# Optimization experiments

Measured on AMD Instinct MI355X. Metric: run time of the kernel, lower is better.

## Reference

```python
import jax, jax.numpy as jnp
import numpy as np

ITERATIONS = 10
EPS = 1e-8
ALPHA = 1.0
BETA = 1.0


def _conv3x3x3(x):
    # all-ones 3x3x3 kernel, padding=1 (SAME), single channel; NCDHW layout
    k = jnp.ones((1, 1, 3, 3, 3), x.dtype)
    return jax.lax.conv_general_dilated(
        x, k, window_strides=(1, 1, 1), padding='SAME',
        dimension_numbers=('NCDHW', 'OIDHW', 'NCDHW'))


def _soft_skeletonize(x):
    x = jax.nn.sigmoid(x)
    skeleton = x
    for _ in range(ITERATIONS):
        eroded = (_conv3x3x3(skeleton) > 0).astype(x.dtype)
        opened = (_conv3x3x3(eroded) > 0).astype(x.dtype)
        skeleton = jnp.clip(skeleton - opened, 0.0, 1.0)
    return skeleton


def _count_components(binary):
    neighbors = _conv3x3x3(binary)
    mask = binary > 0
    cnt = jnp.sum(mask).astype(binary.dtype)
    # torch.mean(neighbors[mask] + eps) == sum((neighbors+eps)*mask)/cnt
    mean_nb = jnp.sum(jnp.where(mask, neighbors + EPS, 0.0)) / jnp.maximum(cnt, 1.0)
    return (cnt / mean_nb)[None]


def setup_inputs() -> dict:
    key = jax.random.key(0)
    k1, k2 = jax.random.split(key)
    pred = jax.random.normal(k1, (2, 1, 192, 192, 192), dtype=jnp.float32)
    target = jax.random.uniform(k2, (2, 1, 192, 192, 192), dtype=jnp.float32)
    return {"pred": pred, "target": target}


def reference(pred, target):
    pred_prob = jax.nn.sigmoid(pred)
    # NOTE: module applies sigmoid again inside _soft_skeletonize (faithful)
    pred_skeleton = _soft_skeletonize(pred_prob)
    target_skeleton = _soft_skeletonize(target)

    intersection = jnp.sum(pred_skeleton * target_skeleton)
    union = jnp.sum(pred_skeleton) + jnp.sum(target_skeleton)
    skeleton_loss = 1.0 - (2.0 * intersection + EPS) / (union + EPS)

    pred_binary = (pred_prob > 0.5).astype(pred.dtype)
    target_binary = target  # .float() no-op
    pred_components = _count_components(pred_binary)
    target_components = _count_components(target_binary)
    connectivity_loss = jnp.mean(jnp.abs(pred_components - target_components))

    return ALPHA * skeleton_loss + BETA * connectivity_loss
```

## Files before the change

kernel.cpp:

```cpp
#include <hip/hip_runtime.h>
#include <math.h>

#define NN 192
#define PLANE (NN * NN)
#define VOLSZ (NN * NN * NN)
#define ZC 24
#define SLABR 8
#define NSLAB (NN / SLABR)
#define SLOTF (10 * NN)
#define NBIN 8
#define EPSF 1e-8f

template <int MODE>
__device__ __forceinline__ float bval(float u) {
  return (MODE == 0) ? ((u > 0.f) ? 1.f : 0.f) : u;
}

#define GLOAD16(G, L)                                                       \
  __builtin_amdgcn_global_load_lds(                                         \
      (const __attribute__((address_space(1))) void*)(G),                   \
      (__attribute__((address_space(3))) void*)(L), 16, 0, 0)

struct PlaneR {
  float4 a, b, c, d;
};

template <int MODE>
__device__ __forceinline__ void consume2(const PlaneR& P, float mA, float mD, float mz,
                                         int lane, float4& sY, float4& sZ,
                                         float4& cY, float4& cZ) {
  const float a0 = bval<MODE>(P.a.x), a1 = bval<MODE>(P.a.y), a2 = bval<MODE>(P.a.z), a3 = bval<MODE>(P.a.w);
  const float b0 = bval<MODE>(P.b.x), b1 = bval<MODE>(P.b.y), b2 = bval<MODE>(P.b.z), b3 = bval<MODE>(P.b.w);
  const float c0 = bval<MODE>(P.c.x), c1 = bval<MODE>(P.c.y), c2 = bval<MODE>(P.c.z), c3 = bval<MODE>(P.c.w);
  const float d0 = bval<MODE>(P.d.x), d1 = bval<MODE>(P.d.y), d2 = bval<MODE>(P.d.z), d3 = bval<MODE>(P.d.w);
  const float u0 = b0 + c0, u1 = b1 + c1, u2 = b2 + c2, u3 = b3 + c3;
  const float tY0 = fmaf(a0, mA, u0), tY1 = fmaf(a1, mA, u1), tY2 = fmaf(a2, mA, u2), tY3 = fmaf(a3, mA, u3);
  const float tZ0 = fmaf(d0, mD, u0), tZ1 = fmaf(d1, mD, u1), tZ2 = fmaf(d2, mD, u2), tZ3 = fmaf(d3, mD, u3);
  const float upY = __shfl_up(tY3, 1), dnY = __shfl_down(tY0, 1);
  const float upZ = __shfl_up(tZ3, 1), dnZ = __shfl_down(tZ0, 1);
  const float tlY = (lane == 0) ? 0.f : upY;
  const float trY = (lane >= 47) ? 0.f : dnY;
  const float tlZ = (lane == 0) ? 0.f : upZ;
  const float trZ = (lane >= 47) ? 0.f : dnZ;
  const float pY01 = tY0 + tY1, pY23 = tY2 + tY3;
  const float pZ01 = tZ0 + tZ1, pZ23 = tZ2 + tZ3;
  sY.x = (tlY + pY01) * mz; sY.y = (pY01 + tY2) * mz; sY.z = (tY1 + pY23) * mz; sY.w = (pY23 + trY) * mz;
  sZ.x = (tlZ + pZ01) * mz; sZ.y = (pZ01 + tZ2) * mz; sZ.z = (tZ1 + pZ23) * mz; sZ.w = (pZ23 + trZ) * mz;
  cY.x = b0; cY.y = b1; cY.z = b2; cY.w = b3;
  cZ.x = c0; cZ.y = c1; cZ.z = c2; cZ.w = c3;
}

#define ACC1(C, SP, SC, SN)                                   \
  {                                                           \
    float m = ((C) > 0.f) ? act : 0.f;                        \
    cnt += m;                                                 \
    acc = fmaf(m, ((SP) + (SC)) + (SN), acc);                 \
  }

#define ACCUM8(snY, snZ)                      \
  ACC1(cY.x, spY.x, scY.x, (snY).x)           \
  ACC1(cY.y, spY.y, scY.y, (snY).y)           \
  ACC1(cY.z, spY.z, scY.z, (snY).z)           \
  ACC1(cY.w, spY.w, scY.w, (snY).w)           \
  ACC1(cZ.x, spZ.x, scZ.x, (snZ).x)           \
  ACC1(cZ.y, spZ.y, scZ.y, (snZ).y)           \
  ACC1(cZ.z, spZ.z, scZ.z, (snZ).z)           \
  ACC1(cZ.w, spZ.w, scZ.w, (snZ).w)

__device__ __forceinline__ void ldsReadP(const float* pl, int slotF, int rbaseF, int xoff, PlaneR& P) {
  const float* p = pl + slotF + rbaseF;
  P.a = *(const float4*)(p + 0 * NN + xoff);
  P.b = *(const float4*)(p + 1 * NN + xoff);
  P.c = *(const float4*)(p + 2 * NN + xoff);
  P.d = *(const float4*)(p + 3 * NN + xoff);
}

__device__ __forceinline__ void issuePlane(const float* __restrict__ base, int z,
                                           int gRow0, float* slotBase, int lane,
                                           int g0F, int g1F, int l0F, int l1F,
                                           int v1e) {
  const int zz = min(max(z, 0), NN - 1);
  const float* gp = base + (size_t)zz * PLANE + gRow0 * NN;
  GLOAD16(gp + g0F, slotBase + l0F);
  if (lane < v1e) GLOAD16(gp + g1F, slotBase + l1F);
}

#define STEPD(RS, WS, DOI, ZLD, MZ, VMASM)                                  \
  {                                                                         \
    asm volatile(VMASM);                                                    \
    __builtin_amdgcn_sched_barrier(0);                                      \
    __builtin_amdgcn_s_barrier();                                           \
    __builtin_amdgcn_sched_barrier(0);                                      \
    if (DOI) issuePlane(base, (ZLD), gRow0, pl + (WS) * SLOTF + shiftF,     \
                        lane, g0F, g1F, l0F, l1F, v1e);                     \
    PlaneR P;                                                               \
    ldsReadP(pl, (RS) * SLOTF, rbaseF, xoff, P);                            \
    float4 snY, snZ, cnY, cnZ;                                              \
    consume2<MODE>(P, mA, mD, (MZ), lane, snY, snZ, cnY, cnZ);              \
    ACCUM8(snY, snZ);                                                       \
    spY = scY; scY = snY; spZ = scZ; scZ = snZ; cY = cnY; cZ = cnZ;         \
  }

template <int MODE>
__device__ __forceinline__ void sweep(const float* __restrict__ base, int y0, int z0,
                                      float* pl, int tid, float& cnt, float& acc) {
  const int lane = tid & 63;
  const int w = tid >> 6;
  const int xoff = 4 * min(lane, 47);
  const float act = (lane < 48) ? 1.f : 0.f;

  const bool loEdge = (y0 == 0), hiEdge = (y0 + SLABR == NN);
  const int gRow0 = loEdge ? 0 : y0 - 1;
  const int nR = 10 - (loEdge ? 1 : 0) - (hiEdge ? 1 : 0);
  const int nQ = nR * 48;
  const int shiftF = loEdge ? NN : 0;

  const int c1 = 4 + w;
  const int v1 = nQ - 64 * c1;
  const int c1e = (v1 > 0) ? c1 : 0;
  const int v1e = (v1 > 0) ? (v1 < 64 ? v1 : 64) : 64;
  const int l0F = 256 * w;
  const int l1F = 256 * c1e;
  const int g0F = 4 * (64 * w + lane);
  const int g1F = 4 * (64 * c1e + lane);

  const int rbaseF = (2 * w) * NN;
  const float mA = (y0 + 2 * w > 0) ? 1.f : 0.f;
  const float mD = (y0 + 2 * w + 2 < NN) ? 1.f : 0.f;
  const float mzLo = (z0 > 0) ? 1.f : 0.f;
  const float mzHi = (z0 + ZC < NN) ? 1.f : 0.f;

  if (loEdge && tid < 48) {
    const float4 z4 = make_float4(0.f, 0.f, 0.f, 0.f);
#pragma unroll
    for (int r = 0; r < 4; ++r) *(float4*)(pl + r * SLOTF + 4 * tid) = z4;
  }
  if (hiEdge && tid < 48) {
    const float4 z4 = make_float4(0.f, 0.f, 0.f, 0.f);
#pragma unroll
    for (int r = 0; r < 4; ++r) *(float4*)(pl + r * SLOTF + 9 * NN + 4 * tid) = z4;
  }

  issuePlane(base, z0 - 1, gRow0, pl + 0 * SLOTF + shiftF, lane, g0F, g1F, l0F, l1F, v1e);
  issuePlane(base, z0,     gRow0, pl + 1 * SLOTF + shiftF, lane, g0F, g1F, l0F, l1F, v1e);
  issuePlane(base, z0 + 1, gRow0, pl + 2 * SLOTF + shiftF, lane, g0F, g1F, l0F, l1F, v1e);
  issuePlane(base, z0 + 2, gRow0, pl + 3 * SLOTF + shiftF, lane, g0F, g1F, l0F, l1F, v1e);
  __syncthreads();

  float4 spY, scY, spZ, scZ, cY, cZ;
  {
    PlaneR P; float4 j1, j2;
    ldsReadP(pl, 0 * SLOTF, rbaseF, xoff, P);
    consume2<MODE>(P, mA, mD, mzLo, lane, spY, spZ, j1, j2);
    ldsReadP(pl, 1 * SLOTF, rbaseF, xoff, P);
    consume2<MODE>(P, mA, mD, 1.f, lane, scY, scZ, cY, cZ);
  }

  {
    asm volatile("s_waitcnt vmcnt(4)");
    __builtin_amdgcn_sched_barrier(0);
    __builtin_amdgcn_s_barrier();
    __builtin_amdgcn_sched_barrier(0);
    issuePlane(base, z0 + 3, gRow0, pl + 0 * SLOTF + shiftF, lane, g0F, g1F, l0F, l1F, v1e);
    issuePlane(base, z0 + 4, gRow0, pl + 1 * SLOTF + shiftF, lane, g0F, g1F, l0F, l1F, v1e);
    PlaneR P;
    ldsReadP(pl, 2 * SLOTF, rbaseF, xoff, P);
    float4 snY, snZ, cnY, cnZ;
    consume2<MODE>(P, mA, mD, 1.f, lane, snY, snZ, cnY, cnZ);
    ACCUM8(snY, snZ);
    spY = scY; scY = snY; spZ = scZ; scZ = snZ; cY = cnY; cZ = cnZ;
  }

#pragma unroll 1
  for (int k = 0; k < 5; ++k) {
    const int zb = z0 + 4 * k;
    STEPD(3, 2, true, zb + 5, 1.f, "s_waitcnt vmcnt(4)");
    STEPD(0, 3, true, zb + 6, 1.f, "s_waitcnt vmcnt(4)");
    STEPD(1, 0, true, zb + 7, 1.f, "s_waitcnt vmcnt(4)");
    STEPD(2, 1, true, zb + 8, 1.f, "s_waitcnt vmcnt(4)");
  }
  STEPD(3, 0, false, 0, 1.f,  "s_waitcnt vmcnt(4)");
  STEPD(0, 0, false, 0, 1.f,  "s_waitcnt vmcnt(2)");
  STEPD(1, 0, false, 0, mzHi, "s_waitcnt vmcnt(0)");
}

__global__ void init_ws(float* __restrict__ ws) {
  if (threadIdx.x < NBIN * 16) ws[threadIdx.x] = 0.f;
}

__global__ __launch_bounds__(256, 1) void skel_main(const float* __restrict__ pred,
                                                    const float* __restrict__ target,
                                                    float* __restrict__ ws) {
  __shared__ float pl[4 * SLOTF];
  const int b = blockIdx.x;
  const int xcd = b & 7;
  const int s = b >> 3;
  const int vol = s / NSLAB;
  const int slab = s % NSLAB;
  const int z0 = xcd * ZC;
  const int y0 = slab * SLABR;
  const float* base = (vol < 2 ? pred : target) + (size_t)(vol & 1) * VOLSZ;
  const int tid = threadIdx.x;

  float cnt = 0.f, acc = 0.f;
  if (vol < 2) sweep<0>(base, y0, z0, pl, tid, cnt, acc);
  else         sweep<1>(base, y0, z0, pl, tid, cnt, acc);

#pragma unroll
  for (int o = 32; o > 0; o >>= 1) {
    cnt += __shfl_down(cnt, o);
    acc += __shfl_down(acc, o);
  }
  __syncthreads();
  if ((tid & 63) == 0) { pl[tid >> 6] = cnt; pl[4 + (tid >> 6)] = acc; }
  __syncthreads();
  if (tid == 0) {
    const int off = (vol < 2) ? 0 : 2;
    float* sp = &ws[((slab & (NBIN - 1)) << 4) + off];
    atomicAdd(sp + 0, pl[0] + pl[1] + pl[2] + pl[3]);
    atomicAdd(sp + 1, pl[4] + pl[5] + pl[6] + pl[7]);
  }
}

__global__ void finalize(const float* __restrict__ ws, float* __restrict__ out) {
  if (threadIdx.x == 0 && blockIdx.x == 0) {
    float cp = 0.f, ap = 0.f, ct = 0.f, at = 0.f;
#pragma unroll
    for (int i = 0; i < NBIN; ++i) {
      cp += ws[i * 16 + 0];
      ap += ws[i * 16 + 1];
      ct += ws[i * 16 + 2];
      at += ws[i * 16 + 3];
    }
    float mp = (ap + EPSF * cp) / fmaxf(cp, 1.f);
    float Pc = cp / mp;
    float mt = (at + EPSF * ct) / fmaxf(ct, 1.f);
    float Tc = ct / mt;
    out[0] = fabsf(Pc - Tc);
  }
}

extern "C" void kernel_launch(void* const* d_in, const int* in_sizes, int n_in,
                              void* d_out, int out_size, void* d_ws, size_t ws_size,
                              hipStream_t stream) {
  const float* pred = (const float*)d_in[0];
  const float* target = (const float*)d_in[1];
  float* ws = (float*)d_ws;
  float* out = (float*)d_out;

  init_ws<<<1, 128, 0, stream>>>(ws);
  skel_main<<<dim3(768), dim3(256), 0, stream>>>(pred, target, ws);
  finalize<<<1, 64, 0, stream>>>(ws, out);
}
```

Baseline: 133.1 us.

## Deepen LDS plane ring to six slots and process two planes per barrier

Grows the shared-memory plane ring buffer from four to six slots and restructures the z-sweep so each barrier step issues two plane loads and consumes two planes. This halves the number of workgroup barriers and waitcnt stalls per sweep and keeps more global-to-LDS loads in flight. In exchange it uses more LDS per block and puts more work between synchronisation points. The prologue, steady-state loop and tail are rescheduled to match the new slot rotation.

Result: no change. 132.9 us (-0.2%).

```diff
diff --git a/kernel.cpp b/kernel.cpp
--- a/kernel.cpp
+++ b/kernel.cpp
@@ -8,6 +8,7 @@
 #define SLABR 8
 #define NSLAB (NN / SLABR)
 #define SLOTF (10 * NN)
+#define NSLOT 6
 #define NBIN 8
 #define EPSF 1e-8f
 
@@ -85,20 +86,30 @@
   if (lane < v1e) GLOAD16(gp + g1F, slotBase + l1F);
 }
 
-#define STEPD(RS, WS, DOI, ZLD, MZ, VMASM)                                  \
+#define CONSUME_SLOT(SS, MZ)                                                \
+  {                                                                         \
+    PlaneR P;                                                               \
+    ldsReadP(pl, (SS) * SLOTF, rbaseF, xoff, P);                            \
+    float4 snY, snZ, cnY, cnZ;                                              \
+    consume2<MODE>(P, mA, mD, (MZ), lane, snY, snZ, cnY, cnZ);              \
+    ACCUM8(snY, snZ);                                                       \
+    spY = scY; scY = snY; spZ = scZ; scZ = snZ; cY = cnY; cZ = cnZ;         \
+  }
+
+#define STEP2(SA, SB, WA, WB, DOI, ZA, ZB, MZB, VMASM)                      \
   {                                                                         \
     asm volatile(VMASM);                                                    \
     __builtin_amdgcn_sched_barrier(0);                                      \
     __builtin_amdgcn_s_barrier();                                           \
     __builtin_amdgcn_sched_barrier(0);                                      \
-    if (DOI) issuePlane(base, (ZLD), gRow0, pl + (WS) * SLOTF + shiftF,     \
-                        lane, g0F, g1F, l0F, l1F, v1e);                     \
-    PlaneR P;                                                               \
-    ldsReadP(pl, (RS) * SLOTF, rbaseF, xoff, P);                            \
-    float4 snY, snZ, cnY, cnZ;                                              \
-    consume2<MODE>(P, mA, mD, (MZ), lane, snY, snZ, cnY, cnZ);              \
-    ACCUM8(snY, snZ);                                                       \
-    spY = scY; scY = snY; spZ = scZ; scZ = snZ; cY = cnY; cZ = cnZ;         \
+    if (DOI) {                                                              \
+      issuePlane(base, (ZA), gRow0, pl + (WA) * SLOTF + shiftF,             \
+                 lane, g0F, g1F, l0F, l1F, v1e);                            \
+      issuePlane(base, (ZB), gRow0, pl + (WB) * SLOTF + shiftF,             \
+                 lane, g0F, g1F, l0F, l1F, v1e);                            \
+    }                                                                       \
+    CONSUME_SLOT(SA, 1.f);                                                  \
+    CONSUME_SLOT(SB, (MZB));                                                \
   }
 
 template <int MODE>
@@ -133,12 +144,12 @@
   if (loEdge && tid < 48) {
     const float4 z4 = make_float4(0.f, 0.f, 0.f, 0.f);
 #pragma unroll
-    for (int r = 0; r < 4; ++r) *(float4*)(pl + r * SLOTF + 4 * tid) = z4;
+    for (int r = 0; r < NSLOT; ++r) *(float4*)(pl + r * SLOTF + 4 * tid) = z4;
   }
   if (hiEdge && tid < 48) {
     const float4 z4 = make_float4(0.f, 0.f, 0.f, 0.f);
 #pragma unroll
-    for (int r = 0; r < 4; ++r) *(float4*)(pl + r * SLOTF + 9 * NN + 4 * tid) = z4;
+    for (int r = 0; r < NSLOT; ++r) *(float4*)(pl + r * SLOTF + 9 * NN + 4 * tid) = z4;
   }
 
   issuePlane(base, z0 - 1, gRow0, pl + 0 * SLOTF + shiftF, lane, g0F, g1F, l0F, l1F, v1e);
@@ -155,33 +166,19 @@
     ldsReadP(pl, 1 * SLOTF, rbaseF, xoff, P);
     consume2<MODE>(P, mA, mD, 1.f, lane, scY, scZ, cY, cZ);
   }
-
-  {
-    asm volatile("s_waitcnt vmcnt(4)");
-    __builtin_amdgcn_sched_barrier(0);
-    __builtin_amdgcn_s_barrier();
-    __builtin_amdgcn_sched_barrier(0);
-    issuePlane(base, z0 + 3, gRow0, pl + 0 * SLOTF + shiftF, lane, g0F, g1F, l0F, l1F, v1e);
-    issuePlane(base, z0 + 4, gRow0, pl + 1 * SLOTF + shiftF, lane, g0F, g1F, l0F, l1F, v1e);
-    PlaneR P;
-    ldsReadP(pl, 2 * SLOTF, rbaseF, xoff, P);
-    float4 snY, snZ, cnY, cnZ;
-    consume2<MODE>(P, mA, mD, 1.f, lane, snY, snZ, cnY, cnZ);
-    ACCUM8(snY, snZ);
-    spY = scY; scY = snY; spZ = scZ; scZ = snZ; cY = cnY; cZ = cnZ;
-  }
+  issuePlane(base, z0 + 3, gRow0, pl + 4 * SLOTF + shiftF, lane, g0F, g1F, l0F, l1F, v1e);
+  issuePlane(base, z0 + 4, gRow0, pl + 5 * SLOTF + shiftF, lane, g0F, g1F, l0F, l1F, v1e);
 
 #pragma unroll 1
-  for (int k = 0; k < 5; ++k) {
-    const int zb = z0 + 4 * k;
-    STEPD(3, 2, true, zb + 5, 1.f, "s_waitcnt vmcnt(4)");
-    STEPD(0, 3, true, zb + 6, 1.f, "s_waitcnt vmcnt(4)");
-    STEPD(1, 0, true, zb + 7, 1.f, "s_waitcnt vmcnt(4)");
-    STEPD(2, 1, true, zb + 8, 1.f, "s_waitcnt vmcnt(4)");
-  }
-  STEPD(3, 0, false, 0, 1.f,  "s_waitcnt vmcnt(4)");
-  STEPD(0, 0, false, 0, 1.f,  "s_waitcnt vmcnt(2)");
-  STEPD(1, 0, false, 0, mzHi, "s_waitcnt vmcnt(0)");
+  for (int k3 = 0; k3 < 3; ++k3) {
+    const int zb = z0 + 6 * k3;
+    STEP2(2, 3, 0, 1, true, zb + 5,  zb + 6,  1.f, "s_waitcnt vmcnt(4)");
+    STEP2(4, 5, 2, 3, true, zb + 7,  zb + 8,  1.f, "s_waitcnt vmcnt(4)");
+    STEP2(0, 1, 4, 5, true, zb + 9,  zb + 10, 1.f, "s_waitcnt vmcnt(4)");
+  }
+  STEP2(2, 3, 0, 1, true,  z0 + 23, z0 + 24, 1.f,  "s_waitcnt vmcnt(4)");
+  STEP2(4, 5, 0, 0, false, 0,       0,       1.f,  "s_waitcnt vmcnt(4)");
+  STEP2(0, 1, 0, 0, false, 0,       0,       mzHi, "s_waitcnt vmcnt(0)");
 }
 
 __global__ void init_ws(float* __restrict__ ws) {
@@ -191,7 +188,7 @@
 __global__ __launch_bounds__(256, 1) void skel_main(const float* __restrict__ pred,
                                                     const float* __restrict__ target,
                                                     float* __restrict__ ws) {
-  __shared__ float pl[4 * SLOTF];
+  __shared__ float pl[NSLOT * SLOTF];
   const int b = blockIdx.x;
   const int xcd = b & 7;
   const int s = b >> 3;
```
